# Kernel tuning notes

Hardware: AMD Instinct MI355X
Metric: run time of the kernel (lower is better)

## Reference

```python
import math
import jax, jax.numpy as jnp
import numpy as np

H, CH, PQ, PV = 12, 16, 4, 8   # heads, c_hidden, qk points, v points
CS, CZ = 384, 128
INF, EPS = 1e5, 1e-8

def _random_rotations(key, shape):
    m = jax.random.normal(key, shape + (3, 3), jnp.float32)
    q, r = jnp.linalg.qr(m)
    d = jnp.sign(jnp.diagonal(r, axis1=-2, axis2=-1))
    q = q * d[..., None, :]
    det = jnp.linalg.det(q)
    return q.at[..., :, 0].multiply(det[..., None])  # proper rotations, det=+1

def setup_inputs() -> dict:
    key = jax.random.key(0)
    ks = jax.random.split(key, 16)
    B, N = 1, 512
    s = jax.random.normal(ks[0], (B, N, CS), jnp.float32)
    z = jax.random.normal(ks[1], (B, N, N, CZ), jnp.float32)
    rot = _random_rotations(ks[2], (B, N))
    trans = 10.0 * jax.random.normal(ks[3], (B, N, 3), jnp.float32)
    mask = jnp.ones((B, N), jnp.float32)
    w = lambda k, i, o: 0.02 * jax.random.normal(k, (i, o), jnp.float32)
    hc = H * CH
    out_dim = H * (CZ + CH + PV * 4)
    return {
        "s": s, "z": z, "rot": rot, "trans": trans, "mask": mask,
        "Wq": w(ks[4], CS, hc), "bq": jnp.zeros((hc,), jnp.float32),
        "Wkv": w(ks[5], CS, 2 * hc), "bkv": jnp.zeros((2 * hc,), jnp.float32),
        "Wqp": w(ks[6], CS, H * PQ * 3), "bqp": jnp.zeros((H * PQ * 3,), jnp.float32),
        "Wkvp": w(ks[7], CS, H * (PQ + PV) * 3), "bkvp": jnp.zeros((H * (PQ + PV) * 3,), jnp.float32),
        "Wb": w(ks[8], CZ, H), "bb": jnp.zeros((H,), jnp.float32),
        "head_weights": jnp.full((H,), float(np.log(np.e - 1.0)), jnp.float32),  # softplus^-1(1)
        "Wout": w(ks[9], out_dim, CS), "bout": jnp.zeros((CS,), jnp.float32),
    }

def reference(s, z, rot, trans, mask, Wq, bq, Wkv, bkv, Wqp, bqp, Wkvp, bkvp, Wb, bb, head_weights, Wout, bout):
    B, N, _ = s.shape
    # scalar q/k/v
    q = (s @ Wq + bq).reshape(B, N, H, CH)
    kv = (s @ Wkv + bkv).reshape(B, N, H, 2 * CH)
    k, v = kv[..., :CH], kv[..., CH:]
    # point projections in local frames, lifted to global via rigid apply
    def proj_pts(W, b, P):
        p = s @ W + b                                    # [B,N,3*H*P] (x|y|z blocks)
        p = jnp.stack(jnp.split(p, 3, axis=-1), axis=-1) # [B,N,H*P,3]
        p = jnp.einsum('bnxy,bnpy->bnpx', rot, p) + trans[:, :, None, :]
        return p.reshape(B, N, H, P, 3)
    q_pts = proj_pts(Wqp, bqp, PQ)
    kv_pts = proj_pts(Wkvp, bkvp, PQ + PV)
    k_pts, v_pts = kv_pts[..., :PQ, :], kv_pts[..., PQ:, :]
    # scalar attention + pair bias
    b_pair = z @ Wb + bb                                 # [B,i,j,H]
    a = jnp.einsum('bihc,bjhc->bhij', q, k) * math.sqrt(1.0 / (3 * CH))
    a = a + math.sqrt(1.0 / 3) * jnp.transpose(b_pair, (0, 3, 1, 2))
    # point distance attention
    d2 = jnp.sum((q_pts[:, :, None] - k_pts[:, None]) ** 2, axis=-1)  # [B,i,j,H,P]
    hw = jax.nn.softplus(head_weights) * math.sqrt(1.0 / (3 * (PQ * 9.0 / 2)))
    pt_att = -0.5 * jnp.sum(d2 * hw[None, None, None, :, None], axis=-1)  # [B,i,j,H]
    a = a + jnp.transpose(pt_att, (0, 3, 1, 2))
    sq_mask = INF * (mask[:, :, None] * mask[:, None, :] - 1.0)
    a = jax.nn.softmax(a + sq_mask[:, None], axis=-1)    # [B,H,i,j]
    # value aggregation
    o = jnp.einsum('bhij,bjhc->bihc', a, v).reshape(B, N, H * CH)
    o_pt = jnp.einsum('bhij,bjhpx->bihpx', a, v_pts)     # [B,N,H,PV,3]
    o_pt = jnp.einsum('bnyx,bnhpy->bnhpx', rot, o_pt - trans[:, :, None, None, :])  # invert_apply
    o_pt_norm = jnp.sqrt(jnp.sum(o_pt ** 2, axis=-1) + EPS).reshape(B, N, H * PV)
    o_pt_f = o_pt.reshape(B, N, H * PV, 3)
    o_pair = jnp.einsum('bhij,bijc->bihc', a, z).reshape(B, N, H * CZ)
    cat = jnp.concatenate([o, o_pt_f[..., 0], o_pt_f[..., 1], o_pt_f[..., 2], o_pt_norm, o_pair], axis=-1)
    return cat @ Wout + bout
```

## Files before the change

### kernel.cpp

```cpp
#include <hip/hip_runtime.h>
#include <hip/hip_bf16.h>

typedef __hip_bfloat16 bf16h;
typedef short bf16x8 __attribute__((ext_vector_type(8)));
typedef float f32x4 __attribute__((ext_vector_type(4)));

#define NH 12
#define CHD 16
#define PQN 4
#define PVN 8
#define CSD 384
#define CZD 128
#define NN 512
#define HC 192
#define OUTD 2112
#define NSQ (NN*NN)
#define NPROJ 1152

#define OFF_Q    0u
#define OFF_K    98304u
#define OFF_V    196608u
#define OFF_QP   294912u
#define OFF_KP   368640u
#define OFF_VP   442368u
#define OFF_RAW  589824u
#define OFF_SB   1179648u
#define OFF_WCT  1277952u
#define OFF_CATB 3735552u
#define OFF_WOT  4276224u
#define OFF_BCAT 4681728u

#define NT_WCT  432
#define NT_WOUT 792
#define WCAT_BLOCKS (NT_WCT + NT_WOUT + 128 + 1)

__global__ __launch_bounds__(256) void k_wcat(
    const float* __restrict__ s,
    const float* __restrict__ Wq, const float* __restrict__ bq,
    const float* __restrict__ Wkv, const float* __restrict__ bkv,
    const float* __restrict__ Wqp, const float* __restrict__ bqp,
    const float* __restrict__ Wkvp, const float* __restrict__ bkvp,
    const float* __restrict__ Wout, float* __restrict__ ws)
{
  __shared__ float tile[32][33];
  const int b = blockIdx.x, t = threadIdx.x;
  const int tx = t & 31, ty = t >> 5;
  if (b < NT_WCT) {
    const int ct = b / 12, rt = b % 12;
    const int col0 = ct*32, c0 = rt*32;
    const int col = col0 + tx;
    const float* W; int ld, colW;
    if (col < 192)      { W = Wq;   ld = 192; colW = col; }
    else if (col < 576) { W = Wkv;  ld = 384; colW = col-192; }
    else if (col < 720) { W = Wqp;  ld = 144; colW = col-576; }
    else                { W = Wkvp; ld = 432; colW = col-720; }
    #pragma unroll
    for (int r = 0; r < 4; ++r)
      tile[ty + r*8][tx] = W[(size_t)(c0 + ty + r*8)*ld + colW];
    __syncthreads();
    bf16h* dstW = (bf16h*)(ws + OFF_WCT);
    #pragma unroll
    for (int r = 0; r < 4; ++r) {
      int colL = ty + r*8;
      dstW[(size_t)(col0 + colL)*CSD + c0 + tx] = __float2bfloat16(tile[tx][colL]);
    }
  } else if (b < NT_WCT + NT_WOUT) {
    const int q = b - NT_WCT;
    const int kt = q / 12, nt2 = q % 12;
    const int k0 = kt*32, n0 = nt2*32;
    #pragma unroll
    for (int r = 0; r < 4; ++r)
      tile[ty + r*8][tx] = Wout[(size_t)(k0 + ty + r*8)*CSD + n0 + tx];
    __syncthreads();
    bf16h* woutT = (bf16h*)(ws + OFF_WOT);
    #pragma unroll
    for (int r = 0; r < 4; ++r) {
      int nL = ty + r*8;
      woutT[(size_t)(n0 + nL)*OUTD + k0 + tx] = __float2bfloat16(tile[tx][nL]);
    }
  } else if (b < NT_WCT + NT_WOUT + 128) {
    const int n0 = (b - (NT_WCT + NT_WOUT))*4;
    bf16h* sb = (bf16h*)(ws + OFF_SB);
    for (int idx = t; idx < 4*CSD; idx += 256)
      sb[(size_t)n0*CSD + idx] = __float2bfloat16(s[(size_t)n0*CSD + idx]);
  } else {
    float* bcat = ws + OFF_BCAT;
    for (int o = t; o < NPROJ; o += 256) {
      float v;
      if (o < 192)      v = bq[o];
      else if (o < 576) v = bkv[o-192];
      else if (o < 720) v = bqp[o-576];
      else              v = bkvp[o-720];
      bcat[o] = v;
    }
  }
}

__global__ __launch_bounds__(256) void k_proj_gemm(float* __restrict__ ws)
{
  const bf16h* sb    = (const bf16h*)(ws + OFF_SB);
  const bf16h* wcatT = (const bf16h*)(ws + OFF_WCT);
  float* raw = ws + OFF_RAW;
  const int t = threadIdx.x;
  const int wave = t >> 6, lane = t & 63;
  const int m0 = blockIdx.x*32 + (wave>>1)*16;
  const int n0 = blockIdx.y*32 + (wave&1)*16;
  const int lm = lane & 15, quad = lane >> 4;
  const bf16x8* pa = (const bf16x8*)(sb    + (size_t)(m0+lm)*CSD) + quad;
  const bf16x8* pb = (const bf16x8*)(wcatT + (size_t)(n0+lm)*CSD) + quad;
  f32x4 acc = {0.f, 0.f, 0.f, 0.f};
  #pragma unroll
  for (int kk = 0; kk < CSD/32; ++kk) {
    bf16x8 av = pa[kk*4];
    bf16x8 bv = pb[kk*4];
    acc = __builtin_amdgcn_mfma_f32_16x16x32_bf16(av, bv, acc, 0, 0, 0);
  }
  const int col = n0 + lm;
  #pragma unroll
  for (int r = 0; r < 4; ++r) {
    int row = m0 + quad*4 + r;
    raw[(size_t)row*NPROJ + col] = acc[r];
  }
}

#define RPB 4
__global__ __launch_bounds__(256) void k_proj_epi(
    const float* __restrict__ rot, const float* __restrict__ trans,
    float* __restrict__ ws)
{
  __shared__ float praw[RPB][576];
  const int n0 = blockIdx.x*RPB, t = threadIdx.x;
  const float* raw = ws + OFF_RAW;
  const float* bcat = ws + OFF_BCAT;
  for (int idx = t; idx < RPB*NPROJ; idx += 256) {
    int r = idx / NPROJ, o = idx - r*NPROJ;
    int n = n0 + r;
    float v = raw[(size_t)n*NPROJ + o] + bcat[o];
    if (o < 192) {
      ws[OFF_Q + n*HC + o] = v;
    } else if (o < 576) {
      int col = o-192, h = col >> 5, rr = col & 31;
      if (rr < CHD) ws[OFF_K + n*HC + h*CHD + rr] = v;
      else          ws[OFF_V + n*HC + h*CHD + (rr-CHD)] = v;
    } else {
      praw[r][o-576] = v;
    }
  }
  __syncthreads();
  for (int m2 = t; m2 < RPB*192; m2 += 256) {
    int r = m2 / 192, m = m2 % 192;
    int n = n0 + r;
    float g0, g1, g2; float* dst;
    if (m < 48) {
      g0 = praw[r][m]; g1 = praw[r][48+m]; g2 = praw[r][96+m];
      int h = m >> 2, p = m & 3;
      dst = ws + OFF_QP + ((n*NH+h)*PQN + p)*3;
    } else {
      int mm = m - 48;
      g0 = praw[r][144+mm]; g1 = praw[r][288+mm]; g2 = praw[r][432+mm];
      int h = mm / 12, pp = mm % 12;
      if (pp < PQN) dst = ws + OFF_KP + ((n*NH+h)*PQN + pp)*3;
      else          dst = ws + OFF_VP + ((n*NH+h)*PVN + (pp-PQN))*3;
    }
    #pragma unroll
    for (int x = 0; x < 3; ++x)
      dst[x] = rot[n*9+x*3+0]*g0 + rot[n*9+x*3+1]*g1 + rot[n*9+x*3+2]*g2 + trans[n*3+x];
  }
}

__global__ __launch_bounds__(512) void k_row(
    const float* __restrict__ z, const float* __restrict__ Wb, const float* __restrict__ bbp,
    const float* __restrict__ mask, const float* __restrict__ head_w,
    const float* __restrict__ rot, const float* __restrict__ trans,
    float* __restrict__ ws)
{
  __shared__ float uzt[512*17];
  __shared__ float ql[HC];
  __shared__ float qpl[144];
  __shared__ float hwl[NH];
  __shared__ float redM[NH][8];
  __shared__ float redS[NH][8];
  __shared__ float optl[288];
  const int t = threadIdx.x, i = blockIdx.x;
  const int wave = t >> 6, lane = t & 63;

  if (t < HC)           ql[t]     = ws[OFF_Q  + (size_t)i*HC  + t];
  else if (t < HC+144)  qpl[t-HC] = ws[OFF_QP + (size_t)i*144 + (t-HC)];
  else if (t >= 352 && t < 352+NH)
    hwl[t-352] = log1pf(expf(head_w[t-352])) * 0.13608276348795434f;

  float acc[NH];
  #pragma unroll
  for (int h = 0; h < NH; ++h) acc[h] = bbp[h];
  float4 pf[4];
  #pragma unroll
  for (int k = 0; k < 4; ++k) {
    int idx4 = k*512 + t;
    int row = idx4 >> 2, c4 = idx4 & 3;
    pf[k] = *(const float4*)(z + ((size_t)i*NN + row)*CZD + c4*4);
  }
  for (int cb = 0; cb < 8; ++cb) {
    __syncthreads();
    #pragma unroll
    for (int k = 0; k < 4; ++k) {
      int idx4 = k*512 + t;
      int row = idx4 >> 2, c4 = idx4 & 3;
      float* d = uzt + row*17 + c4*4;
      d[0]=pf[k].x; d[1]=pf[k].y; d[2]=pf[k].z; d[3]=pf[k].w;
    }
    __syncthreads();
    if (cb < 7) {
      #pragma unroll
      for (int k = 0; k < 4; ++k) {
        int idx4 = k*512 + t;
        int row = idx4 >> 2, c4 = idx4 & 3;
        pf[k] = *(const float4*)(z + ((size_t)i*NN + row)*CZD + (cb+1)*16 + c4*4);
      }
    }
    #pragma unroll
    for (int c = 0; c < 16; ++c) {
      float v = uzt[t*17 + c];
      const float* w = Wb + (cb*16+c)*NH;
      #pragma unroll
      for (int h = 0; h < NH; ++h) acc[h] += v*w[h];
    }
  }

  const float sc13  = 0.57735026918962576f;
  const float sc_qk = 0.14433756729740643f;
  const float mbias = 100000.0f*(mask[i]*mask[t] - 1.0f);
  #define AL(h,j) uzt[(h)*520 + (j)]
  for (int g = 0; g < 3; ++g) {
    float sc4[4];
    #pragma unroll
    for (int u = 0; u < 4; ++u) {
      const int h = g*4 + u;
      const f32x4* kr4 = (const f32x4*)(ws + OFF_K + (size_t)t*HC + h*CHD);
      const f32x4* qr4 = (const f32x4*)(ql + h*CHD);
      float dot = 0.f;
      #pragma unroll
      for (int v4 = 0; v4 < 4; ++v4) {
        f32x4 kv = kr4[v4], qv = qr4[v4];
        dot += qv[0]*kv[0] + qv[1]*kv[1] + qv[2]*kv[2] + qv[3]*kv[3];
      }
      const f32x4* kp4 = (const f32x4*)(ws + OFF_KP + (size_t)t*144 + h*12);
      const f32x4* qp4 = (const f32x4*)(qpl + h*12);
      float d2 = 0.f;
      #pragma unroll
      for (int v4 = 0; v4 < 3; ++v4) {
        f32x4 kv = kp4[v4], qv = qp4[v4];
        float d0 = qv[0]-kv[0], d1 = qv[1]-kv[1], dd2 = qv[2]-kv[2], d3 = qv[3]-kv[3];
        d2 += d0*d0 + d1*d1 + dd2*dd2 + d3*d3;
      }
      float scv = dot*sc_qk + acc[h]*sc13 - 0.5f*hwl[h]*d2 + mbias;
      float mv = scv;
      for (int off = 32; off > 0; off >>= 1) mv = fmaxf(mv, __shfl_xor(mv, off));
      if (lane == 0) redM[h][wave] = mv;
      sc4[u] = scv;
    }
    __syncthreads();
    #pragma unroll
    for (int u = 0; u < 4; ++u) {
      const int h = g*4 + u;
      float mv = redM[h][0];
      #pragma unroll
      for (int w = 1; w < 8; ++w) mv = fmaxf(mv, redM[h][w]);
      float e = expf(sc4[u] - mv);
      sc4[u] = e;
      float sv = e;
      for (int off = 32; off > 0; off >>= 1) sv += __shfl_xor(sv, off);
      if (lane == 0) redS[h][wave] = sv;
    }
    __syncthreads();
    #pragma unroll
    for (int u = 0; u < 4; ++u) {
      const int h = g*4 + u;
      float sv = redS[h][0];
      #pragma unroll
      for (int w = 1; w < 8; ++w) sv += redS[h][w];
      AL(h, t) = sc4[u]*(1.0f/sv);
    }
  }
  __syncthreads();

  {
    const int hg = t >> 7, c = t & 127;
    const int h0 = hg*3;
    float oa0 = 0.f, oa1 = 0.f, oa2 = 0.f;
    const float* zrow = z + ((size_t)i*NN)*CZD + c;
    #pragma unroll 2
    for (int jj = 0; jj < NN; jj += 4) {
      f32x4 a0 = *(const f32x4*)(&AL(h0+0, jj));
      f32x4 a1 = *(const f32x4*)(&AL(h0+1, jj));
      f32x4 a2 = *(const f32x4*)(&AL(h0+2, jj));
      float z0 = zrow[(size_t)(jj+0)*CZD];
      float z1 = zrow[(size_t)(jj+1)*CZD];
      float z2 = zrow[(size_t)(jj+2)*CZD];
      float z3 = zrow[(size_t)(jj+3)*CZD];
      oa0 += a0[0]*z0 + a0[1]*z1 + a0[2]*z2 + a0[3]*z3;
      oa1 += a1[0]*z0 + a1[1]*z1 + a1[2]*z2 + a1[3]*z3;
      oa2 += a2[0]*z0 + a2[1]*z1 + a2[2]*z2 + a2[3]*z3;
    }
    bf16h* dst = (bf16h*)(ws + OFF_CATB) + (size_t)i*OUTD + 576;
    dst[(h0+0)*CZD + c] = __float2bfloat16(oa0);
    dst[(h0+1)*CZD + c] = __float2bfloat16(oa1);
    dst[(h0+2)*CZD + c] = __float2bfloat16(oa2);
  }

  {
    float ob = 0.f;
    int hsel = 0, off = 0, stride = 0;
    const float* src = ws;
    if (t < 192)      { hsel = t >> 4;      src = ws + OFF_V;  off = t;     stride = HC;  }
    else if (t < 480) { hsel = (t-192)/24;  src = ws + OFF_VP; off = t-192; stride = 288; }
    if (t < 480) {
      #pragma unroll 2
      for (int jj = 0; jj < NN; jj += 4) {
        f32x4 av = *(const f32x4*)(&AL(hsel, jj));
        float v0 = src[(size_t)(jj+0)*stride + off];
        float v1 = src[(size_t)(jj+1)*stride + off];
        float v2 = src[(size_t)(jj+2)*stride + off];
        float v3 = src[(size_t)(jj+3)*stride + off];
        ob += av[0]*v0 + av[1]*v1 + av[2]*v2 + av[3]*v3;
      }
    }
    bf16h* catb = (bf16h*)(ws + OFF_CATB);
    if (t < 192)      catb[(size_t)i*OUTD + t] = __float2bfloat16(ob);
    else if (t < 480) optl[t-192] = ob;
    __syncthreads();
    if (t < 96) {
      const int m = t, h = m >> 3;
      float g[3], Tl[3];
      #pragma unroll
      for (int y = 0; y < 3; ++y) { g[y] = optl[h*24 + (m&7)*3 + y]; Tl[y] = trans[i*3+y]; }
      float nrm = 1e-8f;
      float loc[3];
      #pragma unroll
      for (int x = 0; x < 3; ++x) {
        float v = 0.f;
        #pragma unroll
        for (int y = 0; y < 3; ++y) v += rot[i*9 + y*3 + x] * (g[y]-Tl[y]);
        loc[x] = v; nrm += v*v;
      }
      nrm = sqrtf(nrm);
      bf16h* crow = catb + (size_t)i*OUTD;
      crow[192 + 0*96 + m] = __float2bfloat16(loc[0]);
      crow[192 + 1*96 + m] = __float2bfloat16(loc[1]);
      crow[192 + 2*96 + m] = __float2bfloat16(loc[2]);
      crow[480 + m]        = __float2bfloat16(nrm);
    }
  }
  #undef AL
}

__global__ __launch_bounds__(256) void k_out_mfma(
    const float* __restrict__ bout, const float* __restrict__ ws_c, float* __restrict__ out)
{
  const bf16h* catb  = (const bf16h*)(ws_c + OFF_CATB);
  const bf16h* woutT = (const bf16h*)(ws_c + OFF_WOT);
  const int t = threadIdx.x;
  const int wave = t >> 6, lane = t & 63;
  const int m0 = blockIdx.x*32 + (wave>>1)*16;
  const int n0 = blockIdx.y*32 + (wave&1)*16;
  const int lm = lane & 15, quad = lane >> 4;
  const bf16x8* pa = (const bf16x8*)(catb  + (size_t)(m0+lm)*OUTD) + quad;
  const bf16x8* pb = (const bf16x8*)(woutT + (size_t)(n0+lm)*OUTD) + quad;
  f32x4 acc = {0.f, 0.f, 0.f, 0.f};
  #pragma unroll 4
  for (int kk = 0; kk < OUTD/32; ++kk) {
    bf16x8 av = pa[kk*4];
    bf16x8 bv = pb[kk*4];
    acc = __builtin_amdgcn_mfma_f32_16x16x32_bf16(av, bv, acc, 0, 0, 0);
  }
  const int col = n0 + lm;
  const float bb = bout[col];
  #pragma unroll
  for (int r = 0; r < 4; ++r) {
    int row = m0 + quad*4 + r;
    out[(size_t)row*CSD + col] = acc[r] + bb;
  }
}

extern "C" void kernel_launch(void* const* d_in, const int* in_sizes, int n_in,
                              void* d_out, int out_size, void* d_ws, size_t ws_size,
                              hipStream_t stream)
{
  const float* s     = (const float*)d_in[0];
  const float* z     = (const float*)d_in[1];
  const float* rot   = (const float*)d_in[2];
  const float* trans = (const float*)d_in[3];
  const float* mask  = (const float*)d_in[4];
  const float* Wq    = (const float*)d_in[5];
  const float* bq    = (const float*)d_in[6];
  const float* Wkv   = (const float*)d_in[7];
  const float* bkv   = (const float*)d_in[8];
  const float* Wqp   = (const float*)d_in[9];
  const float* bqp   = (const float*)d_in[10];
  const float* Wkvp  = (const float*)d_in[11];
  const float* bkvp  = (const float*)d_in[12];
  const float* Wb    = (const float*)d_in[13];
  const float* bb    = (const float*)d_in[14];
  const float* hwts  = (const float*)d_in[15];
  const float* Wout  = (const float*)d_in[16];
  const float* bout  = (const float*)d_in[17];
  float* ws  = (float*)d_ws;
  float* out = (float*)d_out;

  hipLaunchKernelGGL(k_wcat, dim3(WCAT_BLOCKS), dim3(256), 0, stream,
                     s, Wq, bq, Wkv, bkv, Wqp, bqp, Wkvp, bkvp, Wout, ws);
  hipLaunchKernelGGL(k_proj_gemm, dim3(NN/32, NPROJ/32), dim3(256), 0, stream, ws);
  hipLaunchKernelGGL(k_proj_epi,  dim3(NN/RPB), dim3(256), 0, stream, rot, trans, ws);
  hipLaunchKernelGGL(k_row, dim3(NN), dim3(512), 0, stream,
                     z, Wb, bb, mask, hwts, rot, trans, ws);
  hipLaunchKernelGGL(k_out_mfma, dim3(NN/32, CSD/32), dim3(256), 0, stream, bout, ws, out);
}
```

Before: 352.5 us.

## Double-buffer z tile in k_row and fuse pair/value aggregation loops

The z-bias staging buffer in k_row becomes a double-buffered dynamic LDS region with stride 18. One barrier per chunk is removed and reads and writes use float2. The separate pair-value and scalar/point-value aggregation loops are merged into one loop over j with 8-wide unrolling, so attention weights and loads are issued together. This raises LDS use per block (about 72KB dynamic) and register pressure, which may reduce occupancy. The AL alias for uzt still covers the attention buffer, now in the dynamic region.

After: 374.3 us. +6.2%, slower.

```diff
diff --git a/kernel.cpp b/kernel.cpp
--- a/kernel.cpp
+++ b/kernel.cpp
@@ -33,6 +33,9 @@
 #define NT_WCT  432
 #define NT_WOUT 792
 #define WCAT_BLOCKS (NT_WCT + NT_WOUT + 128 + 1)
+
+#define ZTS 18
+#define KROW_LDS_BYTES (2*512*ZTS*4)
 
 __global__ __launch_bounds__(256) void k_wcat(
     const float* __restrict__ s,
@@ -174,7 +177,7 @@
     const float* __restrict__ rot, const float* __restrict__ trans,
     float* __restrict__ ws)
 {
-  __shared__ float uzt[512*17];
+  extern __shared__ float uzt[];
   __shared__ float ql[HC];
   __shared__ float qpl[144];
   __shared__ float hwl[NH];
@@ -200,15 +203,15 @@
     pf[k] = *(const float4*)(z + ((size_t)i*NN + row)*CZD + c4*4);
   }
   for (int cb = 0; cb < 8; ++cb) {
-    __syncthreads();
+    float* ztw = uzt + (cb & 1)*(512*ZTS);
     #pragma unroll
     for (int k = 0; k < 4; ++k) {
       int idx4 = k*512 + t;
       int row = idx4 >> 2, c4 = idx4 & 3;
-      float* d = uzt + row*17 + c4*4;
-      d[0]=pf[k].x; d[1]=pf[k].y; d[2]=pf[k].z; d[3]=pf[k].w;
-    }
-    __syncthreads();
+      float* d = ztw + row*ZTS + c4*4;
+      *(float2*)(d)     = make_float2(pf[k].x, pf[k].y);
+      *(float2*)(d + 2) = make_float2(pf[k].z, pf[k].w);
+    }
     if (cb < 7) {
       #pragma unroll
       for (int k = 0; k < 4; ++k) {
@@ -217,12 +220,14 @@
         pf[k] = *(const float4*)(z + ((size_t)i*NN + row)*CZD + (cb+1)*16 + c4*4);
       }
     }
-    #pragma unroll
-    for (int c = 0; c < 16; ++c) {
-      float v = uzt[t*17 + c];
-      const float* w = Wb + (cb*16+c)*NH;
-      #pragma unroll
-      for (int h = 0; h < NH; ++h) acc[h] += v*w[h];
+    __syncthreads();
+    const float* ztr = ztw;
+    #pragma unroll
+    for (int c2 = 0; c2 < 8; ++c2) {
+      float2 v = *(const float2*)(ztr + t*ZTS + c2*2);
+      const float* w0 = Wb + (cb*16 + c2*2)*NH;
+      #pragma unroll
+      for (int h = 0; h < NH; ++h) acc[h] += v.x*w0[h] + v.y*w0[NH+h];
     }
   }
 
@@ -284,47 +289,42 @@
   __syncthreads();
 
   {
-    const int hg = t >> 7, c = t & 127;
-    const int h0 = hg*3;
-    float oa0 = 0.f, oa1 = 0.f, oa2 = 0.f;
+    const int hg = t >> 7, c = t & 127, h0 = hg*3;
+    int hsel, off, stride; const float* src;
+    if (t < 192)      { hsel = t >> 4;      src = ws + OFF_V;  off = t;     stride = HC;  }
+    else if (t < 480) { hsel = (t-192)/24;  src = ws + OFF_VP; off = t-192; stride = 288; }
+    else              { hsel = 0;           src = ws + OFF_V;  off = 0;     stride = HC;  }
+    float oa0 = 0.f, oa1 = 0.f, oa2 = 0.f, ob = 0.f;
     const float* zrow = z + ((size_t)i*NN)*CZD + c;
     #pragma unroll 2
-    for (int jj = 0; jj < NN; jj += 4) {
-      f32x4 a0 = *(const f32x4*)(&AL(h0+0, jj));
-      f32x4 a1 = *(const f32x4*)(&AL(h0+1, jj));
-      f32x4 a2 = *(const f32x4*)(&AL(h0+2, jj));
-      float z0 = zrow[(size_t)(jj+0)*CZD];
-      float z1 = zrow[(size_t)(jj+1)*CZD];
-      float z2 = zrow[(size_t)(jj+2)*CZD];
-      float z3 = zrow[(size_t)(jj+3)*CZD];
-      oa0 += a0[0]*z0 + a0[1]*z1 + a0[2]*z2 + a0[3]*z3;
-      oa1 += a1[0]*z0 + a1[1]*z1 + a1[2]*z2 + a1[3]*z3;
-      oa2 += a2[0]*z0 + a2[1]*z1 + a2[2]*z2 + a2[3]*z3;
-    }
-    bf16h* dst = (bf16h*)(ws + OFF_CATB) + (size_t)i*OUTD + 576;
+    for (int jj = 0; jj < NN; jj += 8) {
+      f32x4 p00 = *(const f32x4*)(&AL(h0+0, jj));
+      f32x4 p01 = *(const f32x4*)(&AL(h0+0, jj+4));
+      f32x4 p10 = *(const f32x4*)(&AL(h0+1, jj));
+      f32x4 p11 = *(const f32x4*)(&AL(h0+1, jj+4));
+      f32x4 p20 = *(const f32x4*)(&AL(h0+2, jj));
+      f32x4 p21 = *(const f32x4*)(&AL(h0+2, jj+4));
+      f32x4 pb0 = *(const f32x4*)(&AL(hsel, jj));
+      f32x4 pb1 = *(const f32x4*)(&AL(hsel, jj+4));
+      float zv[8], vv[8];
+      #pragma unroll
+      for (int k2 = 0; k2 < 8; ++k2) zv[k2] = zrow[(size_t)(jj+k2)*CZD];
+      #pragma unroll
+      for (int k2 = 0; k2 < 8; ++k2) vv[k2] = src[(size_t)(jj+k2)*stride + off];
+      oa0 += p00[0]*zv[0]+p00[1]*zv[1]+p00[2]*zv[2]+p00[3]*zv[3]
+           + p01[0]*zv[4]+p01[1]*zv[5]+p01[2]*zv[6]+p01[3]*zv[7];
+      oa1 += p10[0]*zv[0]+p10[1]*zv[1]+p10[2]*zv[2]+p10[3]*zv[3]
+           + p11[0]*zv[4]+p11[1]*zv[5]+p11[2]*zv[6]+p11[3]*zv[7];
+      oa2 += p20[0]*zv[0]+p20[1]*zv[1]+p20[2]*zv[2]+p20[3]*zv[3]
+           + p21[0]*zv[4]+p21[1]*zv[5]+p21[2]*zv[6]+p21[3]*zv[7];
+      ob  += pb0[0]*vv[0]+pb0[1]*vv[1]+pb0[2]*vv[2]+pb0[3]*vv[3]
+           + pb1[0]*vv[4]+pb1[1]*vv[5]+pb1[2]*vv[6]+pb1[3]*vv[7];
+    }
+    bf16h* catb = (bf16h*)(ws + OFF_CATB);
+    bf16h* dst = catb + (size_t)i*OUTD + 576;
     dst[(h0+0)*CZD + c] = __float2bfloat16(oa0);
     dst[(h0+1)*CZD + c] = __float2bfloat16(oa1);
     dst[(h0+2)*CZD + c] = __float2bfloat16(oa2);
-  }
-
-  {
-    float ob = 0.f;
-    int hsel = 0, off = 0, stride = 0;
-    const float* src = ws;
-    if (t < 192)      { hsel = t >> 4;      src = ws + OFF_V;  off = t;     stride = HC;  }
-    else if (t < 480) { hsel = (t-192)/24;  src = ws + OFF_VP; off = t-192; stride = 288; }
-    if (t < 480) {
-      #pragma unroll 2
-      for (int jj = 0; jj < NN; jj += 4) {
-        f32x4 av = *(const f32x4*)(&AL(hsel, jj));
-        float v0 = src[(size_t)(jj+0)*stride + off];
-        float v1 = src[(size_t)(jj+1)*stride + off];
-        float v2 = src[(size_t)(jj+2)*stride + off];
-        float v3 = src[(size_t)(jj+3)*stride + off];
-        ob += av[0]*v0 + av[1]*v1 + av[2]*v2 + av[3]*v3;
-      }
-    }
-    bf16h* catb = (bf16h*)(ws + OFF_CATB);
     if (t < 192)      catb[(size_t)i*OUTD + t] = __float2bfloat16(ob);
     else if (t < 480) optl[t-192] = ob;
     __syncthreads();
@@ -410,7 +410,7 @@
                      s, Wq, bq, Wkv, bkv, Wqp, bqp, Wkvp, bkvp, Wout, ws);
   hipLaunchKernelGGL(k_proj_gemm, dim3(NN/32, NPROJ/32), dim3(256), 0, stream, ws);
   hipLaunchKernelGGL(k_proj_epi,  dim3(NN/RPB), dim3(256), 0, stream, rot, trans, ws);
-  hipLaunchKernelGGL(k_row, dim3(NN), dim3(512), 0, stream,
+  hipLaunchKernelGGL(k_row, dim3(NN), dim3(512), KROW_LDS_BYTES, stream,
                      z, Wb, bb, mask, hwts, rot, trans, ws);
   hipLaunchKernelGGL(k_out_mfma, dim3(NN/32, CSD/32), dim3(256), 0, stream, bout, ws, out);
 }
```
